# Kernel optimization log

Measured on AMD Instinct MI355X. Metric: run time of the kernel, lower is better.

Reference implementation:

```python
import jax, jax.numpy as jnp
import numpy as np
import math

N = 10000      # nodes per type
DIN = 64       # input feature dim
HID = 128      # hidden_dim
HEADS = 8      # num_heads
DH = 128       # per-head dim == out_channels (PyG TransformerConv)
INNER = HEADS * DH  # 1024
L = 2          # num_layers
E = 60000      # edges per edge type
FF = 512       # 4*hidden
LN_EPS = 1e-5


def setup_inputs():
    keys = iter(jax.random.split(jax.random.key(0), 80))
    def mk(shape, std=0.05):
        return std * jax.random.normal(next(keys), shape, dtype=jnp.float32)
    inp = {}
    for t in ("job", "mach"):
        inp[f"x_{t}"] = mk((N, DIN), 1.0)
        inp[f"Win_{t}"] = mk((DIN, HID)); inp[f"bin_{t}"] = mk((HID,), 0.01)
        inp[f"pos_{t}"] = mk((N, HID)); inp[f"te_{t}"] = mk((HID,))
        inp[f"lng_{t}"] = 1.0 + mk((L, HID), 0.02); inp[f"lnb_{t}"] = mk((L, HID), 0.02)
        inp[f"W1_{t}"] = mk((L, HID, FF)); inp[f"b1_{t}"] = mk((L, FF), 0.01)
        inp[f"W2_{t}"] = mk((L, FF, HID)); inp[f"b2_{t}"] = mk((L, HID), 0.01)
        inp[f"Wout_{t}"] = mk((HID, HID)); inp[f"bout_{t}"] = mk((HID,), 0.01)
    for et in ("jm", "mj"):
        inp[f"Wq_{et}"] = mk((L, HID, INNER)); inp[f"Wk_{et}"] = mk((L, HID, INNER))
        inp[f"Wv_{et}"] = mk((L, HID, INNER)); inp[f"Ws_{et}"] = mk((L, HID, HID))
        inp[f"Wb_{et}"] = mk((L, 3 * HID, 1))
        inp[f"bq_{et}"] = mk((L, INNER), 0.01); inp[f"bk_{et}"] = mk((L, INNER), 0.01)
        inp[f"bv_{et}"] = mk((L, INNER), 0.01); inp[f"bs_{et}"] = mk((L, HID), 0.01)
        inp[f"ei_{et}"] = jax.random.randint(next(keys), (2, E), 0, N, dtype=jnp.int32)
    return inp


def _layer_norm(x, g, b):
    mu = x.mean(-1, keepdims=True)
    var = ((x - mu) ** 2).mean(-1, keepdims=True)
    return (x - mu) / jnp.sqrt(var + LN_EPS) * g + b


def _tconv(x_src, x_dst, src, dst, Wq, bq, Wk, bk, Wv, bv, Ws, bs, Wb):
    # PyG TransformerConv(heads=HEADS, out_channels=DH, concat=False, beta=True, root_weight=True)
    Nd = x_dst.shape[0]
    q = (x_dst @ Wq + bq).reshape(Nd, HEADS, DH)
    k = (x_src @ Wk + bk).reshape(-1, HEADS, DH)
    v = (x_src @ Wv + bv).reshape(-1, HEADS, DH)
    logits = jnp.einsum('ehd,ehd->eh', q[dst], k[src]) / math.sqrt(DH)  # [E,H]
    # segment softmax over edges grouped by destination node
    m = jax.ops.segment_max(logits, dst, num_segments=Nd)
    m = jnp.where(jnp.isfinite(m), m, 0.0)  # empty segments -> -inf -> 0
    ex = jnp.exp(logits - m[dst])
    den = jax.ops.segment_sum(ex, dst, num_segments=Nd)
    alpha = ex / (den[dst] + 1e-16)
    agg = jax.ops.segment_sum(alpha[:, :, None] * v[src], dst, num_segments=Nd)
    out = agg.mean(axis=1)              # concat=False -> average heads -> [Nd, DH]
    x_r = x_dst @ Ws + bs               # root/skip projection
    beta = jax.nn.sigmoid(jnp.concatenate([out, x_r, out - x_r], axis=-1) @ Wb)  # [Nd,1]
    return beta * x_r + (1.0 - beta) * out


def _ffn_block(h, new, g, b, W1, b1, W2, b2):
    r = _layer_norm(h + new, g, b)
    return r + (jax.nn.gelu(r @ W1 + b1, approximate=False) @ W2 + b2)


def _forward(x_job, Win_job, bin_job, pos_job, te_job, lng_job, lnb_job, W1_job, b1_job, W2_job, b2_job, Wout_job, bout_job, x_mach, Win_mach, bin_mach, pos_mach, te_mach, lng_mach, lnb_mach, W1_mach, b1_mach, W2_mach, b2_mach, Wout_mach, bout_mach, Wq_jm, Wk_jm, Wv_jm, Ws_jm, Wb_jm, bq_jm, bk_jm, bv_jm, bs_jm, ei_jm, Wq_mj, Wk_mj, Wv_mj, Ws_mj, Wb_mj, bq_mj, bk_mj, bv_mj, bs_mj, ei_mj):
    h_j = x_job @ Win_job + bin_job + te_job + pos_job
    h_m = x_mach @ Win_mach + bin_mach + te_mach + pos_mach
    s_jm, d_jm = ei_jm[0], ei_jm[1]  # job -> mach
    s_mj, d_mj = ei_mj[0], ei_mj[1]  # mach -> job
    for l in range(L):
        new_m = _tconv(h_j, h_m, s_jm, d_jm, Wq_jm[l], bq_jm[l], Wk_jm[l], bk_jm[l], Wv_jm[l], bv_jm[l], Ws_jm[l], bs_jm[l], Wb_jm[l])
        new_j = _tconv(h_m, h_j, s_mj, d_mj, Wq_mj[l], bq_mj[l], Wk_mj[l], bk_mj[l], Wv_mj[l], bv_mj[l], Ws_mj[l], bs_mj[l], Wb_mj[l])
        h_j = _ffn_block(h_j, new_j, lng_job[l], lnb_job[l], W1_job[l], b1_job[l], W2_job[l], b2_job[l])
        h_m = _ffn_block(h_m, new_m, lng_mach[l], lnb_mach[l], W1_mach[l], b1_mach[l], W2_mach[l], b2_mach[l])
    return jnp.stack([h_j @ Wout_job + bout_job, h_m @ Wout_mach + bout_mach], axis=0)


def reference(x_job, Win_job, bin_job, pos_job, te_job, lng_job, lnb_job, W1_job, b1_job, W2_job, b2_job, Wout_job, bout_job, x_mach, Win_mach, bin_mach, pos_mach, te_mach, lng_mach, lnb_mach, W1_mach, b1_mach, W2_mach, b2_mach, Wout_mach, bout_mach, Wq_jm, Wk_jm, Wv_jm, Ws_jm, Wb_jm, bq_jm, bk_jm, bv_jm, bs_jm, ei_jm, Wq_mj, Wk_mj, Wv_mj, Ws_mj, Wb_mj, bq_mj, bk_mj, bv_mj, bs_mj, ei_mj):
    return _forward(x_job, Win_job, bin_job, pos_job, te_job, lng_job, lnb_job, W1_job, b1_job, W2_job, b2_job, Wout_job, bout_job, x_mach, Win_mach, bin_mach, pos_mach, te_mach, lng_mach, lnb_mach, W1_mach, b1_mach, W2_mach, b2_mach, Wout_mach, bout_mach, Wq_jm, Wk_jm, Wv_jm, Ws_jm, Wb_jm, bq_jm, bk_jm, bv_jm, bs_jm, ei_jm, Wq_mj, Wk_mj, Wv_mj, Ws_mj, Wb_mj, bq_mj, bk_mj, bv_mj, bs_mj, ei_mj)
```

## Files before the change

### kernel.cpp

```cpp
#include <hip/hip_runtime.h>
#include <hip/hip_bf16.h>

#define NN 10000
#define EE 60000
#define HIDD 128
#define NH 8
#define INNERD 1024
#define FFD 512
#define KVQ 3072

using u16 = unsigned short;
using u32 = unsigned int;

typedef __bf16 bf16x8 __attribute__((ext_vector_type(8)));
typedef float f32x4 __attribute__((ext_vector_type(4)));

__device__ __forceinline__ float u2f(u32 u) { return __uint_as_float(u << 16); }
__device__ __forceinline__ u16 f2b(float f) {
  u32 x = __float_as_uint(f);
  return (u16)((x + 0x7fffu + ((x >> 16) & 1u)) >> 16);
}
__device__ __forceinline__ float gelu_f(float x) {
  return 0.5f * x * (1.0f + erff(x * 0.70710678118654752f));
}

__global__ void detect_k(const u32* __restrict__ xw, int* __restrict__ flag) {
  if (threadIdx.x == 0 && blockIdx.x == 0) {
    int wild = 0;
    for (int i = 0; i < 256; ++i) {
      float v = u2f(xw[i] & 0xffffu);
      if (!(fabsf(v) < 1e4f)) ++wild;
    }
    *flag = (wild > 16) ? 1 : 0;
  }
}

#define NCVT 30
struct CvtArgs { const void* src[NCVT]; int cnt[NCVT]; int ntot; };

__global__ __launch_bounds__(256) void convert_k(CvtArgs a, const int* __restrict__ flag,
                                                 float* __restrict__ dst) {
  const int i = blockIdx.x * 256 + threadIdx.x;
  if (i >= a.ntot) return;
  int t = 0, off = i;
  while (off >= a.cnt[t]) { off -= a.cnt[t]; ++t; }
  const float v = (*flag) ? ((const float*)a.src[t])[off]
                          : u2f(((const u16*)a.src[t])[off]);
  dst[i] = v;
}

struct TT { const void* s; long off; u16* d; int K; int N; };
struct TTab { TT m[20]; };

__global__ __launch_bounds__(256) void transT_k(TTab tt, const int* __restrict__ flag) {
  const TT m = tt.m[blockIdx.z];
  const int n0 = blockIdx.x * 32, k0 = blockIdx.y * 32;
  if (n0 >= m.N || k0 >= m.K) return;
  __shared__ float tile[32][33];
  const int c = threadIdx.x;
  const int f32in = *flag;
  for (int i = threadIdx.y; i < 32; i += 8) {
    const long gi = m.off + (long)(k0 + i) * m.N + n0 + c;
    tile[i][c] = f32in ? ((const float*)m.s)[gi] : u2f(((const u16*)m.s)[gi]);
  }
  __syncthreads();
  for (int i = threadIdx.y; i < 32; i += 8)
    m.d[(size_t)(n0 + i) * m.K + k0 + c] = f2b(tile[c][i]);
}

__global__ __launch_bounds__(256) void hist_k(const int* __restrict__ ei0,
                                              const int* __restrict__ ei1,
                                              int* __restrict__ hist) {
  const int e = blockIdx.x * 256 + threadIdx.x;
  if (e >= EE) return;
  const int et = blockIdx.y;
  const int* ei = et ? ei1 : ei0;
  atomicAdd(&hist[et * NN + ei[EE + e]], 1);
}

__global__ __launch_bounds__(1024) void scan2_k(const int* __restrict__ hist,
                                                int* __restrict__ rowptr,
                                                int* __restrict__ cursor) {
  const int et = blockIdx.x;
  const int* h = hist + et * NN;
  int* rp = rowptr + et * (NN + 1);
  int* cu = cursor + et * NN;
  __shared__ int wsum[16];
  __shared__ int carrySm;
  const int t = threadIdx.x, lane = t & 63, wid = t >> 6;
  if (t == 0) carrySm = 0;
  __syncthreads();
  for (int base = 0; base < NN; base += 1024) {
    const int idx = base + t;
    const int v = (idx < NN) ? h[idx] : 0;
    int x = v;
#pragma unroll
    for (int off = 1; off < 64; off <<= 1) {
      int y = __shfl_up(x, off);
      if (lane >= off) x += y;
    }
    if (lane == 63) wsum[wid] = x;
    __syncthreads();
    if (wid == 0) {
      int s = (lane < 16) ? wsum[lane] : 0;
#pragma unroll
      for (int off = 1; off < 16; off <<= 1) {
        int y = __shfl_up(s, off);
        if (lane >= off) s += y;
      }
      if (lane < 16) wsum[lane] = s;
    }
    __syncthreads();
    const int waveoff = (wid > 0) ? wsum[wid - 1] : 0;
    const int incl = x + waveoff + carrySm;
    if (idx < NN) { rp[idx] = incl - v; cu[idx] = incl - v; }
    __syncthreads();
    if (t == 1023) carrySm = incl;
    __syncthreads();
  }
  if (t == 0) rp[NN] = carrySm;
}

__global__ __launch_bounds__(256) void scat_k(const int* __restrict__ ei0,
                                              const int* __restrict__ ei1,
                                              int* __restrict__ cursor,
                                              int* __restrict__ srcs) {
  const int e = blockIdx.x * 256 + threadIdx.x;
  if (e >= EE) return;
  const int et = blockIdx.y;
  const int* ei = et ? ei1 : ei0;
  const int s = ei[e], d = ei[EE + e];
  const int pos = atomicAdd(&cursor[et * NN + d], 1);
  srcs[et * EE + pos] = s;
}

__global__ __launch_bounds__(128) void embed2_k(
    const void* __restrict__ x0, const float* __restrict__ Win0,
    const float* __restrict__ bin0, const float* __restrict__ te0,
    const void* __restrict__ pos0, float* __restrict__ h0,
    const void* __restrict__ x1, const float* __restrict__ Win1,
    const float* __restrict__ bin1, const float* __restrict__ te1,
    const void* __restrict__ pos1, float* __restrict__ h1,
    const int* __restrict__ flag) {
  const int ty = blockIdx.y;
  const void* x = ty ? x1 : x0;
  const float* Win = ty ? Win1 : Win0;
  const float* bin = ty ? bin1 : bin0;
  const float* te = ty ? te1 : te0;
  const void* pos = ty ? pos1 : pos0;
  float* h = ty ? h1 : h0;
  __shared__ float Ws[64][128];
  __shared__ float xs[16][64];
  const int f32in = *flag;
  const int j = threadIdx.x;
  const int base = blockIdx.x * 16;
  for (int i = 0; i < 64; ++i) Ws[i][j] = Win[i * 128 + j];
  for (int r = 0; r < 8; ++r) {
    int idx = r * 128 + j;
    int row = idx >> 6, k = idx & 63;
    size_t gi = (size_t)(base + row) * 64 + k;
    xs[row][k] = f32in ? ((const float*)x)[gi] : u2f(((const u16*)x)[gi]);
  }
  __syncthreads();
  float bj = bin[j] + te[j];
  for (int row = 0; row < 16; ++row) {
    size_t gi = (size_t)(base + row) * 128 + j;
    float pv = f32in ? ((const float*)pos)[gi] : u2f(((const u16*)pos)[gi]);
    float acc = bj + pv;
#pragma unroll
    for (int k = 0; k < 64; ++k) acc += xs[row][k] * Ws[k][j];
    h[(size_t)(base + row) * 128 + j] = acc;
  }
}

struct MG {
  const float* A; const u16* WT;
  const float* b0; const float* b1; const float* b2;
  const float* add; float* Cf; u16* Cb;
};

template <int ACT, int OUTB, int ADDS>
__global__ __launch_bounds__(256) void mgemm2_k(MG g0, MG g1, int M, int N, int K) {
  const MG g = blockIdx.z ? g1 : g0;
  __shared__ __align__(16) u16 Asl[128][40];
  __shared__ __align__(16) u16 Bsl[64][40];
  const int t = threadIdx.x;
  const int lane = t & 63, wid = t >> 6;
  const int bm = blockIdx.y * 128, bn = blockIdx.x * 64;
  const int rg = lane >> 4, rr = lane & 15;
  f32x4 acc[2][4];
#pragma unroll
  for (int i = 0; i < 2; ++i)
#pragma unroll
    for (int j = 0; j < 4; ++j) acc[i][j] = (f32x4){0.f, 0.f, 0.f, 0.f};
  const int ar = t >> 1;
  const int ah = (t & 1) << 4;
  const int wr = t >> 2;
  const int wk = (t & 3) << 3;

  for (int k0 = 0; k0 < K; k0 += 32) {
    const int garow = bm + ar;
    float4 v0 = {0,0,0,0}, v1 = {0,0,0,0}, v2 = {0,0,0,0}, v3 = {0,0,0,0};
    if (garow < M) {
      const float* ap = g.A + (size_t)garow * K + k0 + ah;
      v0 = *reinterpret_cast<const float4*>(ap);
      v1 = *reinterpret_cast<const float4*>(ap + 4);
      v2 = *reinterpret_cast<const float4*>(ap + 8);
      v3 = *reinterpret_cast<const float4*>(ap + 12);
    }
    u32 pk[8];
    pk[0] = (u32)f2b(v0.x) | ((u32)f2b(v0.y) << 16);
    pk[1] = (u32)f2b(v0.z) | ((u32)f2b(v0.w) << 16);
    pk[2] = (u32)f2b(v1.x) | ((u32)f2b(v1.y) << 16);
    pk[3] = (u32)f2b(v1.z) | ((u32)f2b(v1.w) << 16);
    pk[4] = (u32)f2b(v2.x) | ((u32)f2b(v2.y) << 16);
    pk[5] = (u32)f2b(v2.z) | ((u32)f2b(v2.w) << 16);
    pk[6] = (u32)f2b(v3.x) | ((u32)f2b(v3.y) << 16);
    pk[7] = (u32)f2b(v3.z) | ((u32)f2b(v3.w) << 16);
    uint4 lo = {pk[0], pk[1], pk[2], pk[3]}, hi = {pk[4], pk[5], pk[6], pk[7]};
    *reinterpret_cast<uint4*>(&Asl[ar][ah]) = lo;
    *reinterpret_cast<uint4*>(&Asl[ar][ah + 8]) = hi;
    const uint4 bv = *reinterpret_cast<const uint4*>(g.WT + (size_t)(bn + wr) * K + k0 + wk);
    *reinterpret_cast<uint4*>(&Bsl[wr][wk]) = bv;
    __syncthreads();
    bf16x8 af[2], bfr[4];
#pragma unroll
    for (int mi = 0; mi < 2; ++mi)
      af[mi] = *reinterpret_cast<const bf16x8*>(&Asl[wid * 32 + mi * 16 + rr][rg * 8]);
#pragma unroll
    for (int ni = 0; ni < 4; ++ni)
      bfr[ni] = *reinterpret_cast<const bf16x8*>(&Bsl[ni * 16 + rr][rg * 8]);
#pragma unroll
    for (int mi = 0; mi < 2; ++mi)
#pragma unroll
      for (int ni = 0; ni < 4; ++ni)
        acc[mi][ni] = __builtin_amdgcn_mfma_f32_16x16x32_bf16(af[mi], bfr[ni], acc[mi][ni], 0, 0, 0);
    __syncthreads();
  }
#pragma unroll
  for (int mi = 0; mi < 2; ++mi) {
#pragma unroll
    for (int ni = 0; ni < 4; ++ni) {
      const int col = bn + ni * 16 + rr;
      const int seg = col >> 10;
      const float* bp = (seg == 0) ? g.b0 : ((seg == 1) ? g.b1 : g.b2);
      const float bcol = bp[col & 1023];
#pragma unroll
      for (int r = 0; r < 4; ++r) {
        const int row = bm + wid * 32 + mi * 16 + rg * 4 + r;
        if (row >= M) continue;
        float v = acc[mi][ni][r] + bcol;
        if (ACT == 1) v = gelu_f(v);
        if (ADDS) v += g.add[(size_t)row * N + col];
        if (OUTB) g.Cb[(size_t)row * N + col] = f2b(v);
        else      g.Cf[(size_t)row * N + col] = v;
      }
    }
  }
}

struct VG {
  const float* A; const float* B; const float* bias;
  const float* add; float* Cf; u16* Cb;
};

template <int ACT, int OUTB, int ADDS>
__global__ __launch_bounds__(256) void gemm2_k(VG g0, VG g1, const int* __restrict__ oflag,
                                               int M, int N, int K) {
  const VG g = blockIdx.z ? g1 : g0;
  __shared__ __align__(16) float As[16][64];
  __shared__ __align__(16) float Bs[16][64];
  const int t = threadIdx.x;
  const int tx = t & 15, ty = t >> 4;
  const int bm = blockIdx.y * 64, bn = blockIdx.x * 64;
  float c[4][4] = {{0.f}};
  const int am = t >> 2;
  const int ak = (t & 3) << 2;
  const int bk = t >> 4;
  const int bn4 = (t & 15) << 2;
  for (int k0 = 0; k0 < K; k0 += 16) {
    float4 av = make_float4(0.f, 0.f, 0.f, 0.f);
    const int arow = bm + am;
    if (arow < M) av = *reinterpret_cast<const float4*>(g.A + (size_t)arow * K + k0 + ak);
    As[ak + 0][am] = av.x; As[ak + 1][am] = av.y;
    As[ak + 2][am] = av.z; As[ak + 3][am] = av.w;
    float4 bv = *reinterpret_cast<const float4*>(g.B + (size_t)(k0 + bk) * N + bn + bn4);
    Bs[bk][bn4 + 0] = bv.x; Bs[bk][bn4 + 1] = bv.y;
    Bs[bk][bn4 + 2] = bv.z; Bs[bk][bn4 + 3] = bv.w;
    __syncthreads();
#pragma unroll
    for (int kk = 0; kk < 16; ++kk) {
      float4 a = *reinterpret_cast<const float4*>(&As[kk][ty << 2]);
      float4 b = *reinterpret_cast<const float4*>(&Bs[kk][tx << 2]);
      c[0][0] += a.x * b.x; c[0][1] += a.x * b.y; c[0][2] += a.x * b.z; c[0][3] += a.x * b.w;
      c[1][0] += a.y * b.x; c[1][1] += a.y * b.y; c[1][2] += a.y * b.z; c[1][3] += a.y * b.w;
      c[2][0] += a.z * b.x; c[2][1] += a.z * b.y; c[2][2] += a.z * b.z; c[2][3] += a.z * b.w;
      c[3][0] += a.w * b.x; c[3][1] += a.w * b.y; c[3][2] += a.w * b.z; c[3][3] += a.w * b.w;
    }
    __syncthreads();
  }
  const int f32out = (OUTB == 2) ? *oflag : 0;
#pragma unroll
  for (int i = 0; i < 4; ++i) {
    const int row = bm + (ty << 2) + i;
    if (row >= M) continue;
#pragma unroll
    for (int j = 0; j < 4; ++j) {
      const int col = bn + (tx << 2) + j;
      float v = c[i][j] + g.bias[col];
      if (ACT == 1) v = gelu_f(v);
      if (ADDS) v += g.add[(size_t)row * N + col];
      if (OUTB == 0)      g.Cf[(size_t)row * N + col] = v;
      else if (OUTB == 1) g.Cb[(size_t)row * N + col] = f2b(v);
      else {
        if (f32out) g.Cf[(size_t)row * N + col] = v;
        else        g.Cb[(size_t)row * N + col] = f2b(v);
      }
    }
  }
}

__global__ __launch_bounds__(256) void attn2_k(
    const u16* __restrict__ kvqJ, const u16* __restrict__ kvqM,
    const int* __restrict__ rowptr, const int* __restrict__ srcs,
    float* __restrict__ aggM, float* __restrict__ aggJ) {
  const int et = blockIdx.y;
  const u16* kvqS = et ? kvqM : kvqJ;
  const u16* kvqD = et ? kvqJ : kvqM;
  const int* rp = rowptr + et * (NN + 1);
  const int* sr = srcs + et * EE;
  float* agg = et ? aggJ : aggM;
  const int d = (blockIdx.x * 256 + threadIdx.x) >> 6;
  const int lane = threadIdx.x & 63;
  const u16* qp = kvqD + (size_t)d * KVQ + 2048 + lane * 16;
  uint4 q0 = *reinterpret_cast<const uint4*>(qp);
  uint4 q1 = *reinterpret_cast<const uint4*>(qp + 8);
  float qf[16];
  {
    u32 w[8] = {q0.x, q0.y, q0.z, q0.w, q1.x, q1.y, q1.z, q1.w};
#pragma unroll
    for (int i = 0; i < 8; ++i) { qf[2*i] = u2f(w[i] & 0xffffu); qf[2*i+1] = u2f(w[i] >> 16); }
  }
  float m = -INFINITY, den = 0.f;
  float acc[16];
#pragma unroll
  for (int i = 0; i < 16; ++i) acc[i] = 0.f;
  const int beg = rp[d], end = rp[d + 1];
  for (int idx = beg; idx < end; ++idx) {
    const int s = sr[idx];
    const u16* kp = kvqS + (size_t)s * KVQ + lane * 16;
    uint4 k0 = *reinterpret_cast<const uint4*>(kp);
    uint4 k1 = *reinterpret_cast<const uint4*>(kp + 8);
    uint4 w0 = *reinterpret_cast<const uint4*>(kp + 1024);
    uint4 w1 = *reinterpret_cast<const uint4*>(kp + 1024 + 8);
    float part = 0.f;
    {
      u32 w[8] = {k0.x, k0.y, k0.z, k0.w, k1.x, k1.y, k1.z, k1.w};
#pragma unroll
      for (int i = 0; i < 8; ++i) {
        part += qf[2*i] * u2f(w[i] & 0xffffu);
        part += qf[2*i+1] * u2f(w[i] >> 16);
      }
    }
    part += __shfl_xor(part, 1);
    part += __shfl_xor(part, 2);
    part += __shfl_xor(part, 4);
    const float lg = part * 0.088388347648318447f;
    const float nm = fmaxf(m, lg);
    const float cor = __expf(m - nm);
    const float p = __expf(lg - nm);
    den = den * cor + p;
    float vf[16];
    {
      u32 w[8] = {w0.x, w0.y, w0.z, w0.w, w1.x, w1.y, w1.z, w1.w};
#pragma unroll
      for (int i = 0; i < 8; ++i) { vf[2*i] = u2f(w[i] & 0xffffu); vf[2*i+1] = u2f(w[i] >> 16); }
    }
#pragma unroll
    for (int i = 0; i < 16; ++i) acc[i] = acc[i] * cor + p * vf[i];
    m = nm;
  }
  const float inv = 0.125f / (den + 1e-16f);
  float o[16];
#pragma unroll
  for (int i = 0; i < 16; ++i) {
    float tv = acc[i] * inv;
    tv += __shfl_xor(tv, 8);
    tv += __shfl_xor(tv, 16);
    tv += __shfl_xor(tv, 32);
    o[i] = tv;
  }
  if (lane < 8) {
    float* op = agg + (size_t)d * HIDD + lane * 16;
    *reinterpret_cast<float4*>(op + 0)  = make_float4(o[0],  o[1],  o[2],  o[3]);
    *reinterpret_cast<float4*>(op + 4)  = make_float4(o[4],  o[5],  o[6],  o[7]);
    *reinterpret_cast<float4*>(op + 8)  = make_float4(o[8],  o[9],  o[10], o[11]);
    *reinterpret_cast<float4*>(op + 12) = make_float4(o[12], o[13], o[14], o[15]);
  }
}

struct BL {
  const float* agg; const float* xr; const float* Wb;
  const float* h; const float* g; const float* b; float* r;
};

__global__ __launch_bounds__(256) void betaln2_k(BL p0, BL p1) {
  const BL p = blockIdx.y ? p1 : p0;
  const int n = (blockIdx.x * 256 + threadIdx.x) >> 6;
  const int lane = threadIdx.x & 63;
  const float o0 = p.agg[(size_t)n * HIDD + lane], o1 = p.agg[(size_t)n * HIDD + 64 + lane];
  const float x0 = p.xr[(size_t)n * HIDD + lane], x1 = p.xr[(size_t)n * HIDD + 64 + lane];
  float s = o0 * p.Wb[lane] + o1 * p.Wb[64 + lane]
          + x0 * p.Wb[128 + lane] + x1 * p.Wb[192 + lane]
          + (o0 - x0) * p.Wb[256 + lane] + (o1 - x1) * p.Wb[320 + lane];
#pragma unroll
  for (int mask = 1; mask < 64; mask <<= 1) s += __shfl_xor(s, mask);
  const float beta = 1.f / (1.f + expf(-s));
  const float n0 = beta * x0 + (1.f - beta) * o0;
  const float n1 = beta * x1 + (1.f - beta) * o1;
  const float v0 = p.h[(size_t)n * HIDD + lane] + n0;
  const float v1 = p.h[(size_t)n * HIDD + 64 + lane] + n1;
  float sm = v0 + v1;
#pragma unroll
  for (int mask = 1; mask < 64; mask <<= 1) sm += __shfl_xor(sm, mask);
  const float mu = sm * (1.f / 128.f);
  const float d0 = v0 - mu, d1 = v1 - mu;
  float vs = d0 * d0 + d1 * d1;
#pragma unroll
  for (int mask = 1; mask < 64; mask <<= 1) vs += __shfl_xor(vs, mask);
  const float rstd = rsqrtf(vs * (1.f / 128.f) + 1e-5f);
  p.r[(size_t)n * HIDD + lane]      = d0 * rstd * p.g[lane] + p.b[lane];
  p.r[(size_t)n * HIDD + 64 + lane] = d1 * rstd * p.g[64 + lane] + p.b[64 + lane];
}

extern "C" void kernel_launch(void* const* d_in, const int* in_sizes, int n_in,
                              void* d_out, int out_size, void* d_ws, size_t ws_size,
                              hipStream_t stream) {
  char* w = (char*)d_ws;
  auto carve = [&](size_t bytes) { void* p = (void*)w; w += (bytes + 255) & ~(size_t)255; return p; };
  float* h_b[2];  h_b[0] = (float*)carve((size_t)NN * HIDD * 4); h_b[1] = (float*)carve((size_t)NN * HIDD * 4);
  float* rb_b[2]; rb_b[0] = (float*)carve((size_t)NN * HIDD * 4); rb_b[1] = (float*)carve((size_t)NN * HIDD * 4);
  float* xr_b[2]; xr_b[0] = (float*)carve((size_t)NN * HIDD * 4); xr_b[1] = (float*)carve((size_t)NN * HIDD * 4);
  float* ag_b[2]; ag_b[0] = (float*)carve((size_t)NN * HIDD * 4); ag_b[1] = (float*)carve((size_t)NN * HIDD * 4);
  u16* kvqJ = (u16*)carve((size_t)NN * KVQ * 2);
  u16* kvqM = (u16*)carve((size_t)NN * KVQ * 2);
  float* mid_b[2] = {(float*)kvqJ, (float*)kvqM};
  int* histb  = (int*)carve(2 * NN * 4);
  int* rowptr = (int*)carve(2 * (NN + 1) * 4);
  int* cursor = (int*)carve(2 * NN * 4);
  int* srcsb  = (int*)carve(2 * EE * 4);
  int* flagp  = (int*)carve(256);
  const int totCvt = 2 * 26752 + 2 * 39936;
  float* wf = (float*)carve((size_t)totCvt * 4);
  u16* wtp = (u16*)carve((size_t)2097152 * 2);

  CvtArgs ca; int nc = 0; int cum = 0;
  auto addc = [&](int inIdx, int n) -> float* {
    ca.src[nc] = d_in[inIdx]; ca.cnt[nc] = n; float* p = wf + cum; cum += n; ++nc; return p;
  };
  const float *WinF[2], *binF[2], *teF[2], *lngF[2], *lnbF[2], *b1F[2], *b2F[2], *WoutF[2], *boutF[2];
  const void* x_p[2]; const void* pos_p[2];
  for (int t = 0; t < 2; ++t) {
    const int o = t * 13;
    x_p[t] = d_in[o + 0];
    WinF[t] = addc(o + 1, 64 * HIDD);
    binF[t] = addc(o + 2, HIDD);
    pos_p[t] = d_in[o + 3];
    teF[t]  = addc(o + 4, HIDD);
    lngF[t] = addc(o + 5, 2 * HIDD);
    lnbF[t] = addc(o + 6, 2 * HIDD);
    b1F[t]  = addc(o + 8, 2 * FFD);
    b2F[t]  = addc(o + 10, 2 * HIDD);
    WoutF[t] = addc(o + 11, HIDD * HIDD);
    boutF[t] = addc(o + 12, HIDD);
  }
  const float *WsF[2], *WbF[2], *bqF[2], *bkF[2], *bvF[2], *bsF[2];
  const int* ei_e[2];
  for (int et = 0; et < 2; ++et) {
    const int o = 26 + et * 10;
    WsF[et] = addc(o + 3, 2 * HIDD * HIDD);
    WbF[et] = addc(o + 4, 2 * 384);
    bqF[et] = addc(o + 5, 2 * INNERD);
    bkF[et] = addc(o + 6, 2 * INNERD);
    bvF[et] = addc(o + 7, 2 * INNERD);
    bsF[et] = addc(o + 8, 2 * HIDD);
    ei_e[et] = (const int*)d_in[o + 9];
  }
  ca.ntot = cum;

  TTab tt; int ntt = 0; u16* tcur = wtp;
  auto addT = [&](const void* s, long off, int K, int N, u16* dst) {
    tt.m[ntt] = {s, off, dst, K, N}; ++ntt;
  };
  u16* kvqWT[2][2];
  for (int et = 0; et < 2; ++et) {
    const int o  = 26 + et * 10;
    const int oq = 26 + (1 - et) * 10;
    for (int l = 0; l < 2; ++l) {
      u16* base = tcur; tcur += (size_t)KVQ * HIDD;
      kvqWT[et][l] = base;
      addT(d_in[o + 1],  (long)l * HIDD * INNERD, HIDD, INNERD, base);
      addT(d_in[o + 2],  (long)l * HIDD * INNERD, HIDD, INNERD, base + 1024 * HIDD);
      addT(d_in[oq + 0], (long)l * HIDD * INNERD, HIDD, INNERD, base + 2048 * HIDD);
    }
  }
  u16 *W1T[2][2], *W2T[2][2];
  for (int t = 0; t < 2; ++t) {
    const int o = t * 13;
    for (int l = 0; l < 2; ++l) {
      W1T[t][l] = tcur; addT(d_in[o + 7], (long)l * HIDD * FFD, HIDD, FFD, tcur); tcur += (size_t)HIDD * FFD;
      W2T[t][l] = tcur; addT(d_in[o + 9], (long)l * FFD * HIDD, FFD, HIDD, tcur); tcur += (size_t)FFD * HIDD;
    }
  }

  const dim3 blk(256);
  const int MB64 = (NN + 63) / 64;
  const int MB128 = (NN + 127) / 128;

  detect_k<<<1, 64, 0, stream>>>((const u32*)d_in[0], flagp);
  convert_k<<<(cum + 255) / 256, blk, 0, stream>>>(ca, flagp, wf);
  transT_k<<<dim3(32, 16, 20), dim3(32, 8), 0, stream>>>(tt, flagp);
  hipMemsetAsync(histb, 0, 2 * NN * 4, stream);
  hist_k<<<dim3((EE + 255) / 256, 2), blk, 0, stream>>>(ei_e[0], ei_e[1], histb);
  scan2_k<<<2, 1024, 0, stream>>>(histb, rowptr, cursor);
  scat_k<<<dim3((EE + 255) / 256, 2), blk, 0, stream>>>(ei_e[0], ei_e[1], cursor, srcsb);

  embed2_k<<<dim3(NN / 16, 2), 128, 0, stream>>>(
      x_p[0], WinF[0], binF[0], teF[0], pos_p[0], h_b[0],
      x_p[1], WinF[1], binF[1], teF[1], pos_p[1], h_b[1], flagp);

  for (int l = 0; l < 2; ++l) {
    MG gj = {h_b[0], kvqWT[0][l], bkF[0] + l * INNERD, bvF[0] + l * INNERD,
             bqF[1] + l * INNERD, nullptr, nullptr, kvqJ};
    MG gm = {h_b[1], kvqWT[1][l], bkF[1] + l * INNERD, bvF[1] + l * INNERD,
             bqF[0] + l * INNERD, nullptr, nullptr, kvqM};
    mgemm2_k<0, 1, 0><<<dim3(KVQ / 64, MB128, 2), blk, 0, stream>>>(gj, gm, NN, KVQ, HIDD);
    attn2_k<<<dim3(NN / 4, 2), blk, 0, stream>>>(kvqJ, kvqM, rowptr, srcsb, ag_b[1], ag_b[0]);
    VG vs0 = {h_b[1], WsF[0] + (size_t)l * HIDD * HIDD, bsF[0] + l * HIDD, nullptr, xr_b[1], nullptr};
    VG vs1 = {h_b[0], WsF[1] + (size_t)l * HIDD * HIDD, bsF[1] + l * HIDD, nullptr, xr_b[0], nullptr};
    gemm2_k<0, 0, 0><<<dim3(HIDD / 64, MB64, 2), blk, 0, stream>>>(vs0, vs1, nullptr, NN, HIDD, HIDD);
    BL p0 = {ag_b[1], xr_b[1], WbF[0] + l * 384, h_b[1], lngF[1] + l * HIDD, lnbF[1] + l * HIDD, rb_b[1]};
    BL p1 = {ag_b[0], xr_b[0], WbF[1] + l * 384, h_b[0], lngF[0] + l * HIDD, lnbF[0] + l * HIDD, rb_b[0]};
    betaln2_k<<<dim3(NN / 4, 2), blk, 0, stream>>>(p0, p1);
    MG w1j = {rb_b[0], W1T[0][l], b1F[0] + l * FFD, b1F[0] + l * FFD, b1F[0] + l * FFD,
              nullptr, mid_b[0], nullptr};
    MG w1m = {rb_b[1], W1T[1][l], b1F[1] + l * FFD, b1F[1] + l * FFD, b1F[1] + l * FFD,
              nullptr, mid_b[1], nullptr};
    mgemm2_k<1, 0, 0><<<dim3(FFD / 64, MB128, 2), blk, 0, stream>>>(w1j, w1m, NN, FFD, HIDD);
    MG w2j = {mid_b[0], W2T[0][l], b2F[0] + l * HIDD, b2F[0] + l * HIDD, b2F[0] + l * HIDD,
              rb_b[0], h_b[0], nullptr};
    MG w2m = {mid_b[1], W2T[1][l], b2F[1] + l * HIDD, b2F[1] + l * HIDD, b2F[1] + l * HIDD,
              rb_b[1], h_b[1], nullptr};
    mgemm2_k<0, 0, 1><<<dim3(HIDD / 64, MB128, 2), blk, 0, stream>>>(w2j, w2m, NN, HIDD, FFD);
  }
  VG o0 = {h_b[0], WoutF[0], boutF[0], nullptr, (float*)d_out, (u16*)d_out};
  VG o1 = {h_b[1], WoutF[1], boutF[1], nullptr,
           (float*)d_out + (size_t)NN * HIDD, (u16*)d_out + (size_t)NN * HIDD};
  gemm2_k<0, 2, 0><<<dim3(HIDD / 64, MB64, 2), blk, 0, stream>>>(o0, o1, flagp, NN, HIDD, HIDD);
}
```

Measured before the change: 527.2 us.

## Fuse skip projection into KVQ GEMM, keep bf16 activation copies, unroll attention edges

Appends the root/skip weight Ws as an extra 128 columns to the K/V/Q MFMA GEMM, which removes the separate FP32 gemm2 launch for the skip projection. The embedding, LayerNorm and FFN kernels now also write bf16 copies of their activations. The MFMA GEMMs therefore load bf16 A directly instead of reading FP32 and converting per tile, and the FFN intermediate is stored as bf16. The attention kernel processes two edges per iteration to issue more gather loads concurrently. In exchange there are extra bf16 stores and workspace, and the skip projection and FFN intermediate now run at bf16 precision.

```diff
diff --git a/kernel.cpp b/kernel.cpp
--- a/kernel.cpp
+++ b/kernel.cpp
@@ -8,6 +8,7 @@
 #define INNERD 1024
 #define FFD 512
 #define KVQ 3072
+#define KVQS 3200
 
 using u16 = unsigned short;
 using u32 = unsigned int;
@@ -50,7 +51,7 @@
 }
 
 struct TT { const void* s; long off; u16* d; int K; int N; };
-struct TTab { TT m[20]; };
+struct TTab { TT m[28]; };
 
 __global__ __launch_bounds__(256) void transT_k(TTab tt, const int* __restrict__ flag) {
   const TT m = tt.m[blockIdx.z];
@@ -137,10 +138,10 @@
 __global__ __launch_bounds__(128) void embed2_k(
     const void* __restrict__ x0, const float* __restrict__ Win0,
     const float* __restrict__ bin0, const float* __restrict__ te0,
-    const void* __restrict__ pos0, float* __restrict__ h0,
+    const void* __restrict__ pos0, float* __restrict__ h0, u16* __restrict__ h80,
     const void* __restrict__ x1, const float* __restrict__ Win1,
     const float* __restrict__ bin1, const float* __restrict__ te1,
-    const void* __restrict__ pos1, float* __restrict__ h1,
+    const void* __restrict__ pos1, float* __restrict__ h1, u16* __restrict__ h81,
     const int* __restrict__ flag) {
   const int ty = blockIdx.y;
   const void* x = ty ? x1 : x0;
@@ -149,6 +150,7 @@
   const float* te = ty ? te1 : te0;
   const void* pos = ty ? pos1 : pos0;
   float* h = ty ? h1 : h0;
+  u16* h8 = ty ? h81 : h80;
   __shared__ float Ws[64][128];
   __shared__ float xs[16][64];
   const int f32in = *flag;
@@ -170,16 +172,17 @@
 #pragma unroll
     for (int k = 0; k < 64; ++k) acc += xs[row][k] * Ws[k][j];
     h[(size_t)(base + row) * 128 + j] = acc;
+    h8[(size_t)(base + row) * 128 + j] = f2b(acc);
   }
 }
 
 struct MG {
-  const float* A; const u16* WT;
-  const float* b0; const float* b1; const float* b2;
+  const u16* A; const u16* WT;
+  const float* b0; const float* b1; const float* b2; const float* b3;
   const float* add; float* Cf; u16* Cb;
 };
 
-template <int ACT, int OUTB, int ADDS>
+template <int MODE>
 __global__ __launch_bounds__(256) void mgemm2_k(MG g0, MG g1, int M, int N, int K) {
   const MG g = blockIdx.z ? g1 : g0;
   __shared__ __align__(16) u16 Asl[128][40];
@@ -200,26 +203,14 @@
 
   for (int k0 = 0; k0 < K; k0 += 32) {
     const int garow = bm + ar;
-    float4 v0 = {0,0,0,0}, v1 = {0,0,0,0}, v2 = {0,0,0,0}, v3 = {0,0,0,0};
+    uint4 a0 = {0,0,0,0}, a1 = {0,0,0,0};
     if (garow < M) {
-      const float* ap = g.A + (size_t)garow * K + k0 + ah;
-      v0 = *reinterpret_cast<const float4*>(ap);
-      v1 = *reinterpret_cast<const float4*>(ap + 4);
-      v2 = *reinterpret_cast<const float4*>(ap + 8);
-      v3 = *reinterpret_cast<const float4*>(ap + 12);
-    }
-    u32 pk[8];
-    pk[0] = (u32)f2b(v0.x) | ((u32)f2b(v0.y) << 16);
-    pk[1] = (u32)f2b(v0.z) | ((u32)f2b(v0.w) << 16);
-    pk[2] = (u32)f2b(v1.x) | ((u32)f2b(v1.y) << 16);
-    pk[3] = (u32)f2b(v1.z) | ((u32)f2b(v1.w) << 16);
-    pk[4] = (u32)f2b(v2.x) | ((u32)f2b(v2.y) << 16);
-    pk[5] = (u32)f2b(v2.z) | ((u32)f2b(v2.w) << 16);
-    pk[6] = (u32)f2b(v3.x) | ((u32)f2b(v3.y) << 16);
-    pk[7] = (u32)f2b(v3.z) | ((u32)f2b(v3.w) << 16);
-    uint4 lo = {pk[0], pk[1], pk[2], pk[3]}, hi = {pk[4], pk[5], pk[6], pk[7]};
-    *reinterpret_cast<uint4*>(&Asl[ar][ah]) = lo;
-    *reinterpret_cast<uint4*>(&Asl[ar][ah + 8]) = hi;
+      const u16* ap = g.A + (size_t)garow * K + k0 + ah;
+      a0 = *reinterpret_cast<const uint4*>(ap);
+      a1 = *reinterpret_cast<const uint4*>(ap + 8);
+    }
+    *reinterpret_cast<uint4*>(&Asl[ar][ah]) = a0;
+    *reinterpret_cast<uint4*>(&Asl[ar][ah + 8]) = a1;
     const uint4 bv = *reinterpret_cast<const uint4*>(g.WT + (size_t)(bn + wr) * K + k0 + wk);
     *reinterpret_cast<uint4*>(&Bsl[wr][wk]) = bv;
     __syncthreads();
@@ -242,18 +233,30 @@
 #pragma unroll
     for (int ni = 0; ni < 4; ++ni) {
       const int col = bn + ni * 16 + rr;
-      const int seg = col >> 10;
-      const float* bp = (seg == 0) ? g.b0 : ((seg == 1) ? g.b1 : g.b2);
-      const float bcol = bp[col & 1023];
+      float bcol;
+      if (MODE == 2) {
+        const int seg = col >> 10;
+        const float* bp = (seg == 0) ? g.b0 : ((seg == 1) ? g.b1 : ((seg == 2) ? g.b2 : g.b3));
+        bcol = bp[col & 1023];
+      } else {
+        bcol = g.b0[col];
+      }
 #pragma unroll
       for (int r = 0; r < 4; ++r) {
         const int row = bm + wid * 32 + mi * 16 + rg * 4 + r;
         if (row >= M) continue;
         float v = acc[mi][ni][r] + bcol;
-        if (ACT == 1) v = gelu_f(v);
-        if (ADDS) v += g.add[(size_t)row * N + col];
-        if (OUTB) g.Cb[(size_t)row * N + col] = f2b(v);
-        else      g.Cf[(size_t)row * N + col] = v;
+        if (MODE == 2) {
+          if (col < KVQ) g.Cb[(size_t)row * KVQ + col] = f2b(v);
+          else           g.Cf[(size_t)row * HIDD + (col - KVQ)] = v;
+        } else if (MODE == 3) {
+          v = gelu_f(v);
+          g.Cb[(size_t)row * N + col] = f2b(v);
+        } else {
+          v += g.add[(size_t)row * N + col];
+          g.Cf[(size_t)row * N + col] = v;
+          g.Cb[(size_t)row * N + col] = f2b(v);
+        }
       }
     }
   }
@@ -261,10 +264,9 @@
 
 struct VG {
   const float* A; const float* B; const float* bias;
-  const float* add; float* Cf; u16* Cb;
+  float* Cf; u16* Cb;
 };
 
-template <int ACT, int OUTB, int ADDS>
 __global__ __launch_bounds__(256) void gemm2_k(VG g0, VG g1, const int* __restrict__ oflag,
                                                int M, int N, int K) {
   const VG g = blockIdx.z ? g1 : g0;
@@ -299,7 +301,7 @@
     }
     __syncthreads();
   }
-  const int f32out = (OUTB == 2) ? *oflag : 0;
+  const int f32out = *oflag;
 #pragma unroll
   for (int i = 0; i < 4; ++i) {
     const int row = bm + (ty << 2) + i;
@@ -308,14 +310,8 @@
     for (int j = 0; j < 4; ++j) {
       const int col = bn + (tx << 2) + j;
       float v = c[i][j] + g.bias[col];
-      if (ACT == 1) v = gelu_f(v);
-      if (ADDS) v += g.add[(size_t)row * N + col];
-      if (OUTB == 0)      g.Cf[(size_t)row * N + col] = v;
-      else if (OUTB == 1) g.Cb[(size_t)row * N + col] = f2b(v);
-      else {
-        if (f32out) g.Cf[(size_t)row * N + col] = v;
-        else        g.Cb[(size_t)row * N + col] = f2b(v);
-      }
+      if (f32out) g.Cf[(size_t)row * N + col] = v;
+      else        g.Cb[(size_t)row * N + col] = f2b(v);
     }
   }
 }
@@ -346,22 +342,18 @@
 #pragma unroll
   for (int i = 0; i < 16; ++i) acc[i] = 0.f;
   const int beg = rp[d], end = rp[d + 1];
-  for (int idx = beg; idx < end; ++idx) {
-    const int s = sr[idx];
-    const u16* kp = kvqS + (size_t)s * KVQ + lane * 16;
-    uint4 k0 = *reinterpret_cast<const uint4*>(kp);
-    uint4 k1 = *reinterpret_cast<const uint4*>(kp + 8);
-    uint4 w0 = *reinterpret_cast<const uint4*>(kp + 1024);
-    uint4 w1 = *reinterpret_cast<const uint4*>(kp + 1024 + 8);
-    float part = 0.f;
-    {
-      u32 w[8] = {k0.x, k0.y, k0.z, k0.w, k1.x, k1.y, k1.z, k1.w};
-#pragma unroll
-      for (int i = 0; i < 8; ++i) {
-        part += qf[2*i] * u2f(w[i] & 0xffffu);
-        part += qf[2*i+1] * u2f(w[i] >> 16);
-      }
-    }
+
+  auto dot8 = [&](const uint4& a, const uint4& b) -> float {
+    float p = 0.f;
+    const u32 w[8] = {a.x, a.y, a.z, a.w, b.x, b.y, b.z, b.w};
+#pragma unroll
+    for (int i = 0; i < 8; ++i) {
+      p += qf[2*i] * u2f(w[i] & 0xffffu);
+      p += qf[2*i+1] * u2f(w[i] >> 16);
+    }
+    return p;
+  };
+  auto update = [&](float part, const uint4& v0w, const uint4& v1w) {
     part += __shfl_xor(part, 1);
     part += __shfl_xor(part, 2);
     part += __shfl_xor(part, 4);
@@ -370,16 +362,43 @@
     const float cor = __expf(m - nm);
     const float p = __expf(lg - nm);
     den = den * cor + p;
-    float vf[16];
-    {
-      u32 w[8] = {w0.x, w0.y, w0.z, w0.w, w1.x, w1.y, w1.z, w1.w};
-#pragma unroll
-      for (int i = 0; i < 8; ++i) { vf[2*i] = u2f(w[i] & 0xffffu); vf[2*i+1] = u2f(w[i] >> 16); }
-    }
-#pragma unroll
-    for (int i = 0; i < 16; ++i) acc[i] = acc[i] * cor + p * vf[i];
+    const u32 w[8] = {v0w.x, v0w.y, v0w.z, v0w.w, v1w.x, v1w.y, v1w.z, v1w.w};
+#pragma unroll
+    for (int i = 0; i < 8; ++i) {
+      acc[2*i]   = acc[2*i]   * cor + p * u2f(w[i] & 0xffffu);
+      acc[2*i+1] = acc[2*i+1] * cor + p * u2f(w[i] >> 16);
+    }
     m = nm;
-  }
+  };
+
+  int idx = beg;
+  for (; idx + 2 <= end; idx += 2) {
+    const int s0 = sr[idx], s1 = sr[idx + 1];
+    const u16* kp0 = kvqS + (size_t)s0 * KVQ + lane * 16;
+    const u16* kp1 = kvqS + (size_t)s1 * KVQ + lane * 16;
+    const uint4 a0 = *reinterpret_cast<const uint4*>(kp0);
+    const uint4 a1 = *reinterpret_cast<const uint4*>(kp0 + 8);
+    const uint4 av0 = *reinterpret_cast<const uint4*>(kp0 + 1024);
+    const uint4 av1 = *reinterpret_cast<const uint4*>(kp0 + 1024 + 8);
+    const uint4 b0 = *reinterpret_cast<const uint4*>(kp1);
+    const uint4 b1 = *reinterpret_cast<const uint4*>(kp1 + 8);
+    const uint4 bv0 = *reinterpret_cast<const uint4*>(kp1 + 1024);
+    const uint4 bv1 = *reinterpret_cast<const uint4*>(kp1 + 1024 + 8);
+    const float p0 = dot8(a0, a1);
+    const float p1 = dot8(b0, b1);
+    update(p0, av0, av1);
+    update(p1, bv0, bv1);
+  }
+  if (idx < end) {
+    const int s0 = sr[idx];
+    const u16* kp0 = kvqS + (size_t)s0 * KVQ + lane * 16;
+    const uint4 a0 = *reinterpret_cast<const uint4*>(kp0);
+    const uint4 a1 = *reinterpret_cast<const uint4*>(kp0 + 8);
+    const uint4 av0 = *reinterpret_cast<const uint4*>(kp0 + 1024);
+    const uint4 av1 = *reinterpret_cast<const uint4*>(kp0 + 1024 + 8);
+    update(dot8(a0, a1), av0, av1);
+  }
+
   const float inv = 0.125f / (den + 1e-16f);
   float o[16];
 #pragma unroll
@@ -401,7 +420,7 @@
 
 struct BL {
   const float* agg; const float* xr; const float* Wb;
-  const float* h; const float* g; const float* b; float* r;
+  const float* h; const float* g; const float* b; float* r; u16* r8;
 };
 
 __global__ __launch_bounds__(256) void betaln2_k(BL p0, BL p1) {
@@ -429,8 +448,12 @@
 #pragma unroll
   for (int mask = 1; mask < 64; mask <<= 1) vs += __shfl_xor(vs, mask);
   const float rstd = rsqrtf(vs * (1.f / 128.f) + 1e-5f);
-  p.r[(size_t)n * HIDD + lane]      = d0 * rstd * p.g[lane] + p.b[lane];
-  p.r[(size_t)n * HIDD + 64 + lane] = d1 * rstd * p.g[64 + lane] + p.b[64 + lane];
+  const float r0 = d0 * rstd * p.g[lane] + p.b[lane];
+  const float r1 = d1 * rstd * p.g[64 + lane] + p.b[64 + lane];
+  p.r[(size_t)n * HIDD + lane]      = r0;
+  p.r[(size_t)n * HIDD + 64 + lane] = r1;
+  p.r8[(size_t)n * HIDD + lane]      = f2b(r0);
+  p.r8[(size_t)n * HIDD + 64 + lane] = f2b(r1);
 }
 
 extern "C" void kernel_launch(void* const* d_in, const int* in_sizes, int n_in,
@@ -439,20 +462,22 @@
   char* w = (char*)d_ws;
   auto carve = [&](size_t bytes) { void* p = (void*)w; w += (bytes + 255) & ~(size_t)255; return p; };
   float* h_b[2];  h_b[0] = (float*)carve((size_t)NN * HIDD * 4); h_b[1] = (float*)carve((size_t)NN * HIDD * 4);
+  u16* h8_b[2];   h8_b[0] = (u16*)carve((size_t)NN * HIDD * 2);  h8_b[1] = (u16*)carve((size_t)NN * HIDD * 2);
   float* rb_b[2]; rb_b[0] = (float*)carve((size_t)NN * HIDD * 4); rb_b[1] = (float*)carve((size_t)NN * HIDD * 4);
+  u16* rb8_b[2];  rb8_b[0] = (u16*)carve((size_t)NN * HIDD * 2);  rb8_b[1] = (u16*)carve((size_t)NN * HIDD * 2);
   float* xr_b[2]; xr_b[0] = (float*)carve((size_t)NN * HIDD * 4); xr_b[1] = (float*)carve((size_t)NN * HIDD * 4);
   float* ag_b[2]; ag_b[0] = (float*)carve((size_t)NN * HIDD * 4); ag_b[1] = (float*)carve((size_t)NN * HIDD * 4);
   u16* kvqJ = (u16*)carve((size_t)NN * KVQ * 2);
   u16* kvqM = (u16*)carve((size_t)NN * KVQ * 2);
-  float* mid_b[2] = {(float*)kvqJ, (float*)kvqM};
+  u16* mid8_b[2] = {kvqJ, kvqM};
   int* histb  = (int*)carve(2 * NN * 4);
   int* rowptr = (int*)carve(2 * (NN + 1) * 4);
   int* cursor = (int*)carve(2 * NN * 4);
   int* srcsb  = (int*)carve(2 * EE * 4);
   int* flagp  = (int*)carve(256);
-  const int totCvt = 2 * 26752 + 2 * 39936;
+  const int totCvt = 2 * 26752 + 2 * 7168;
   float* wf = (float*)carve((size_t)totCvt * 4);
-  u16* wtp = (u16*)carve((size_t)2097152 * 2);
+  u16* wtp = (u16*)carve((size_t)(4 * KVQS * HIDD + 8 * HIDD * FFD) * 2);
 
   CvtArgs ca; int nc = 0; int cum = 0;
   auto addc = [&](int inIdx, int n) -> float* {
@@ -474,11 +499,10 @@
     WoutF[t] = addc(o + 11, HIDD * HIDD);
     boutF[t] = addc(o + 12, HIDD);
   }
-  const float *WsF[2], *WbF[2], *bqF[2], *bkF[2], *bvF[2], *bsF[2];
+  const float *WbF[2], *bqF[2], *bkF[2], *bvF[2], *bsF[2];
   const int* ei_e[2];
   for (int et = 0; et < 2; ++et) {
     const int o = 26 + et * 10;
-    WsF[et] = addc(o + 3, 2 * HIDD * HIDD);
     WbF[et] = addc(o + 4, 2 * 384);
     bqF[et] = addc(o + 5, 2 * INNERD);
     bkF[et] = addc(o + 6, 2 * INNERD);
@@ -497,11 +521,12 @@
     const int o  = 26 + et * 10;
     const int oq = 26 + (1 - et) * 10;
     for (int l = 0; l < 2; ++l) {
-      u16* base = tcur; tcur += (size_t)KVQ * HIDD;
+      u16* base = tcur; tcur += (size_t)KVQS * HIDD;
       kvqWT[et][l] = base;
       addT(d_in[o + 1],  (long)l * HIDD * INNERD, HIDD, INNERD, base);
       addT(d_in[o + 2],  (long)l * HIDD * INNERD, HIDD, INNERD, base + 1024 * HIDD);
       addT(d_in[oq + 0], (long)l * HIDD * INNERD, HIDD, INNERD, base + 2048 * HIDD);
+      addT(d_in[oq + 3], (long)l * HIDD * HIDD,   HIDD, HIDD,   base + 3072 * HIDD);
     }
   }
   u16 *W1T[2][2], *W2T[2][2];
@@ -519,42 +544,41 @@
 
   detect_k<<<1, 64, 0, stream>>>((const u32*)d_in[0], flagp);
   convert_k<<<(cum + 255) / 256, blk, 0, stream>>>(ca, flagp, wf);
-  transT_k<<<dim3(32, 16, 20), dim3(32, 8), 0, stream>>>(tt, flagp);
+  transT_k<<<dim3(32, 16, 24), dim3(32, 8), 0, stream>>>(tt, flagp);
   hipMemsetAsync(histb, 0, 2 * NN * 4, stream);
   hist_k<<<dim3((EE + 255) / 256, 2), blk, 0, stream>>>(ei_e[0], ei_e[1], histb);
   scan2_k<<<2, 1024, 0, stream>>>(histb, rowptr, cursor);
   scat_k<<<dim3((EE + 255) / 256, 2), blk, 0, stream>>>(ei_e[0], ei_e[1], cursor, srcsb);
 
   embed2_k<<<dim3(NN / 16, 2), 128, 0, stream>>>(
-      x_p[0], WinF[0], binF[0], teF[0], pos_p[0], h_b[0],
-      x_p[1], WinF[1], binF[1], teF[1], pos_p[1], h_b[1], flagp);
+      x_p[0], WinF[0], binF[0], teF[0], pos_p[0], h_b[0], h8_b[0],
+      x_p[1], WinF[1], binF[1], teF[1], pos_p[1], h_b[1], h8_b[1], flagp);
 
   for (int l = 0; l < 2; ++l) {
-    MG gj = {h_b[0], kvqWT[0][l], bkF[0] + l * INNERD, bvF[0] + l * INNERD,
-             bqF[1] + l * INNERD, nullptr, nullptr, kvqJ};
-    MG gm = {h_b[1], kvqWT[1][l], bkF[1] + l * INNERD, bvF[1] + l * INNERD,
-             bqF[0] + l * INNERD, nullptr, nullptr, kvqM};
-    mgemm2_k<0, 1, 0><<<dim3(KVQ / 64, MB128, 2), blk, 0, stream>>>(gj, gm, NN, KVQ, HIDD);
+    MG gj = {h8_b[0], kvqWT[0][l], bkF[0] + l * INNERD, bvF[0] + l * INNERD,
+             bqF[1] + l * INNERD, bsF[1] + l * HIDD, nullptr, xr_b[0], kvqJ};
+    MG gm = {h8_b[1], kvqWT[1][l], bkF[1] + l * INNERD, bvF[1] + l * INNERD,
+             bqF[0] + l * INNERD, bsF[0] + l * HIDD, nullptr, xr_b[1], kvqM};
+    mgemm2_k<2><<<dim3(KVQS / 64, MB128, 2), blk, 0, stream>>>(gj, gm, NN, KVQS, HIDD);
     attn2_k<<<dim3(NN / 4, 2), blk, 0, stream>>>(kvqJ, kvqM, rowptr, srcsb, ag_b[1], ag_b[0]);
-    VG vs0 = {h_b[1], WsF[0] + (size_t)l * HIDD * HIDD, bsF[0] + l * HIDD, nullptr, xr_b[1], nullptr};
-    VG vs1 = {h_b[0], WsF[1] + (size_t)l * HIDD * HIDD, bsF[1] + l * HIDD, nullptr, xr_b[0], nullptr};
-    gemm2_k<0, 0, 0><<<dim3(HIDD / 64, MB64, 2), blk, 0, stream>>>(vs0, vs1, nullptr, NN, HIDD, HIDD);
-    BL p0 = {ag_b[1], xr_b[1], WbF[0] + l * 384, h_b[1], lngF[1] + l * HIDD, lnbF[1] + l * HIDD, rb_b[1]};
-    BL p1 = {ag_b[0], xr_b[0], WbF[1] + l * 384, h_b[0], lngF[0] + l * HIDD, lnbF[0] + l * HIDD, rb_b[0]};
+    BL p0 = {ag_b[1], xr_b[1], WbF[0] + l * 384, h_b[1],
+             lngF[1] + l * HIDD, lnbF[1] + l * HIDD, rb_b[1], rb8_b[1]};
+    BL p1 = {ag_b[0], xr_b[0], WbF[1] + l * 384, h_b[0],
+             lngF[0] + l * HIDD, lnbF[0] + l * HIDD, rb_b[0], rb8_b[0]};
     betaln2_k<<<dim3(NN / 4, 2), blk, 0, stream>>>(p0, p1);
-    MG w1j = {rb_b[0], W1T[0][l], b1F[0] + l * FFD, b1F[0] + l * FFD, b1F[0] + l * FFD,
-              nullptr, mid_b[0], nullptr};
-    MG w1m = {rb_b[1], W1T[1][l], b1F[1] + l * FFD, b1F[1] + l * FFD, b1F[1] + l * FFD,
-              nullptr, mid_b[1], nullptr};
-    mgemm2_k<1, 0, 0><<<dim3(FFD / 64, MB128, 2), blk, 0, stream>>>(w1j, w1m, NN, FFD, HIDD);
-    MG w2j = {mid_b[0], W2T[0][l], b2F[0] + l * HIDD, b2F[0] + l * HIDD, b2F[0] + l * HIDD,
-              rb_b[0], h_b[0], nullptr};
-    MG w2m = {mid_b[1], W2T[1][l], b2F[1] + l * HIDD, b2F[1] + l * HIDD, b2F[1] + l * HIDD,
-              rb_b[1], h_b[1], nullptr};
-    mgemm2_k<0, 0, 1><<<dim3(HIDD / 64, MB128, 2), blk, 0, stream>>>(w2j, w2m, NN, HIDD, FFD);
-  }
-  VG o0 = {h_b[0], WoutF[0], boutF[0], nullptr, (float*)d_out, (u16*)d_out};
-  VG o1 = {h_b[1], WoutF[1], boutF[1], nullptr,
+    MG w1j = {rb8_b[0], W1T[0][l], b1F[0] + l * FFD, nullptr, nullptr, nullptr,
+              nullptr, nullptr, mid8_b[0]};
+    MG w1m = {rb8_b[1], W1T[1][l], b1F[1] + l * FFD, nullptr, nullptr, nullptr,
+              nullptr, nullptr, mid8_b[1]};
+    mgemm2_k<3><<<dim3(FFD / 64, MB128, 2), blk, 0, stream>>>(w1j, w1m, NN, FFD, HIDD);
+    MG w2j = {mid8_b[0], W2T[0][l], b2F[0] + l * HIDD, nullptr, nullptr, nullptr,
+              rb_b[0], h_b[0], h8_b[0]};
+    MG w2m = {mid8_b[1], W2T[1][l], b2F[1] + l * HIDD, nullptr, nullptr, nullptr,
+              rb_b[1], h_b[1], h8_b[1]};
+    mgemm2_k<4><<<dim3(HIDD / 64, MB128, 2), blk, 0, stream>>>(w2j, w2m, NN, HIDD, FFD);
+  }
+  VG o0 = {h_b[0], WoutF[0], boutF[0], (float*)d_out, (u16*)d_out};
+  VG o1 = {h_b[1], WoutF[1], boutF[1],
            (float*)d_out + (size_t)NN * HIDD, (u16*)d_out + (size_t)NN * HIDD};
-  gemm2_k<0, 2, 0><<<dim3(HIDD / 64, MB64, 2), blk, 0, stream>>>(o0, o1, flagp, NN, HIDD, HIDD);
-}
+  gemm2_k<<<dim3(HIDD / 64, MB64, 2), blk, 0, stream>>>(o0, o1, flagp, NN, HIDD, HIDD);
+}
```

After: 467.2 us. 11.4% less time.
